# Optimization experiments

Measured on AMD Instinct MI355X. Metric: run time of the kernel, lower is better.

The kernel has to match this reference:

```python
import jax, jax.numpy as jnp
import numpy as np

N_NODES = 100000
N_EDGES = 1600000
NFEAT, NHID, NOUT = 128, 64, 32


def setup_inputs() -> dict:
    key = jax.random.key(0)
    ks = jax.random.split(key, 8)
    x = jax.random.normal(ks[0], (N_NODES, NFEAT), dtype=jnp.float32)
    adj_vals = jax.random.uniform(ks[1], (N_EDGES,), dtype=jnp.float32)
    W1 = jax.random.normal(ks[2], (NFEAT, NHID), dtype=jnp.float32) * (1.0 / np.sqrt(NFEAT))
    b1 = jnp.zeros((NHID,), dtype=jnp.float32)
    W2 = jax.random.normal(ks[3], (NHID, NOUT), dtype=jnp.float32) * (1.0 / np.sqrt(NHID))
    b2 = jnp.zeros((NOUT,), dtype=jnp.float32)
    edge_src = jax.random.randint(ks[4], (N_EDGES,), 0, N_NODES, dtype=jnp.int32)
    edge_dst = jax.random.randint(ks[5], (N_EDGES,), 0, N_NODES, dtype=jnp.int32)
    return {"x": x, "adj_vals": adj_vals, "W1": W1, "b1": b1, "W2": W2,
            "b2": b2, "edge_src": edge_src, "edge_dst": edge_dst}


def spmm(vals, src, dst, dense, n_nodes):
    # out[i, :] = sum_{e : dst[e]==i} vals[e] * dense[src[e], :]
    gathered = dense[src] * vals[:, None]          # [E, D] gather (memory-bound)
    return jax.ops.segment_sum(gathered, dst, num_segments=n_nodes)


def reference(x, adj_vals, W1, b1, W2, b2, edge_src, edge_dst):
    # GraphConvolution 1: support = x @ W1; out = adj @ support + b1; relu
    h = spmm(adj_vals, edge_src, edge_dst, x @ W1, N_NODES) + b1
    h = jax.nn.relu(h)
    # dropout is identity in eval mode (training=False)
    # GraphConvolution 2
    out = spmm(adj_vals, edge_src, edge_dst, h @ W2, N_NODES) + b2
    return out
```

## Files before the change

### kernel.cpp

```cpp
#include <hip/hip_runtime.h>
#include <hip/hip_fp16.h>

#define N_NODES 100000
#define N_EDGES 1600000
#define NFEAT 128
#define NHID 64
#define NOUT 32

#define NPB 256
#define NB ((N_NODES + NPB - 1) / NPB)
#define CAP 4608
#define CCH 4096
#define NCH ((N_EDGES + CCH - 1) / CCH)
#define G1B ((N_NODES / 16 + 3) / 4)

typedef _Float16 half8 __attribute__((ext_vector_type(8)));
typedef float floatx4 __attribute__((ext_vector_type(4)));

__device__ __forceinline__ int wave_incl_scan(int v, int lane) {
#pragma unroll
    for (int d = 1; d < 64; d <<= 1) {
        int t = __shfl_up(v, d, 64);
        if (lane >= d) v += t;
    }
    return v;
}
__device__ __forceinline__ int block_excl_scan_256(int tsum, int tid, int* w4) {
    const int lane = tid & 63, wid = tid >> 6;
    int incl = wave_incl_scan(tsum, lane);
    if (lane == 63) w4[wid] = incl;
    __syncthreads();
    int wbase = 0;
    if (wid > 0) wbase += w4[0];
    if (wid > 1) wbase += w4[1];
    if (wid > 2) wbase += w4[2];
    return wbase + incl - tsum;
}

__global__ __launch_bounds__(64) void prep_kernel(const float* __restrict__ W1,
                                                  __half* __restrict__ wfrag,
                                                  int* __restrict__ gcur) {
    const int l = threadIdx.x;
    const int b = blockIdx.x;
    if (b < 16) {
        const int ks = b >> 2, ct = b & 3;
        const int kb = ks * 32 + (l >> 4) * 8;
        const int c  = ct * 16 + (l & 15);
        union { __half2 h2[4]; uint4 u; } pk;
#pragma unroll
        for (int j = 0; j < 4; ++j)
            pk.h2[j] = __floats2half2_rn(W1[(kb + 2 * j) * NHID + c],
                                         W1[(kb + 2 * j + 1) * NHID + c]);
        *(uint4*)&wfrag[((size_t)b * 64 + l) * 8] = pk.u;
    } else {
        int i = (b - 16) * 64 + l;
        if (i < NB) gcur[i] = i * CAP;
    }
}

__global__ __launch_bounds__(256) void g1cs_kernel(const float* __restrict__ x,
                                                   const __half* __restrict__ wfrag,
                                                   __half* __restrict__ support,
                                                   const float* __restrict__ vals,
                                                   const int* __restrict__ src,
                                                   const int* __restrict__ dst,
                                                   int* __restrict__ gcur,
                                                   uint2* __restrict__ recsC) {
    __shared__ int cnt[NB];
    __shared__ int pos[NB];
    const int tid = threadIdx.x;

    if (blockIdx.x < NCH) {
        const int cbase0 = blockIdx.x * CCH;
        for (int i = tid; i < NB; i += 256) cnt[i] = 0;
        int dstv[CCH / 256];
        __syncthreads();
#pragma unroll
        for (int k = 0; k < CCH / 256; ++k) {
            int e = cbase0 + k * 256 + tid;
            int d = (e < N_EDGES) ? dst[e] : -1;
            dstv[k] = d;
            if (d >= 0) atomicAdd(&cnt[d >> 8], 1);
        }
        __syncthreads();
        for (int b = tid; b < NB; b += 256) {
            int c = cnt[b];
            pos[b] = c ? atomicAdd(&gcur[b], c) : 0;
        }
        __syncthreads();
#pragma unroll
        for (int k = 0; k < CCH / 256; ++k) {
            int e = cbase0 + k * 256 + tid;
            int d = dstv[k];
            if (d >= 0) {
                int b = d >> 8;
                int slot = atomicAdd(&pos[b], 1);
                if (slot < (b + 1) * CAP)
                    recsC[slot] = make_uint2((unsigned)src[e] |
                                             ((unsigned)(d & (NPB - 1)) << 17),
                                             __float_as_uint(vals[e]));
            }
        }
    } else {
        const int lane = tid & 63;
        const int tile = (blockIdx.x - NCH) * 4 + (tid >> 6);
        const int n0 = tile * 16;
        if (n0 >= N_NODES) return;

        half8 a[4][4];
#pragma unroll
        for (int ks = 0; ks < 4; ++ks)
#pragma unroll
            for (int ct = 0; ct < 4; ++ct)
                a[ks][ct] = *(const half8*)&wfrag[((size_t)(ks * 4 + ct) * 64 + lane) * 8];

        floatx4 acc[4];
#pragma unroll
        for (int ct = 0; ct < 4; ++ct) acc[ct] = (floatx4){0.f, 0.f, 0.f, 0.f};

        const int node = n0 + (lane & 15);
        const float* xrow = x + (size_t)node * NFEAT + (lane >> 4) * 8;

#pragma unroll
        for (int ks = 0; ks < 4; ++ks) {
            float4 f0 = *(const float4*)(xrow + ks * 32);
            float4 f1 = *(const float4*)(xrow + ks * 32 + 4);
            union { __half2 h2[4]; half8 v; } bv;
            bv.h2[0] = __floats2half2_rn(f0.x, f0.y);
            bv.h2[1] = __floats2half2_rn(f0.z, f0.w);
            bv.h2[2] = __floats2half2_rn(f1.x, f1.y);
            bv.h2[3] = __floats2half2_rn(f1.z, f1.w);
#pragma unroll
            for (int ct = 0; ct < 4; ++ct)
                acc[ct] = __builtin_amdgcn_mfma_f32_16x16x32_f16(a[ks][ct], bv.v, acc[ct], 0, 0, 0);
        }

        __half* srow = support + (size_t)node * NHID + (lane >> 4) * 4;
#pragma unroll
        for (int ct = 0; ct < 4; ++ct) {
            union { __half2 h2[2]; uint2 u; } pk;
            pk.h2[0] = __floats2half2_rn(acc[ct][0], acc[ct][1]);
            pk.h2[1] = __floats2half2_rn(acc[ct][2], acc[ct][3]);
            *(uint2*)&srow[ct * 16] = pk.u;
        }
    }
}

__global__ __launch_bounds__(256) void fine_sort_kernel(const int* __restrict__ gcur,
                                                        const uint2* __restrict__ recsC,
                                                        uint2* __restrict__ recs2,
                                                        int* __restrict__ offs,
                                                        int* __restrict__ ends) {
    __shared__ int cnt[NPB];
    __shared__ int cur[NPB];
    __shared__ int w4[4];
    const int tid = threadIdx.x;
    const int b = blockIdx.x;
    const int s = b * CAP;
    const int e = min(gcur[b], s + CAP);
    cnt[tid] = 0;
    __syncthreads();
    for (int i = s + tid; i < e; i += 256)
        atomicAdd(&cnt[(recsC[i].x >> 17) & (NPB - 1)], 1);
    __syncthreads();
    int v = cnt[tid];
    int excl = block_excl_scan_256(v, tid, w4);
    cur[tid] = excl;
    const int node = b * NPB + tid;
    if (node < N_NODES) {
        offs[node] = s + excl;
        ends[node] = s + excl + v;
    }
    __syncthreads();
    for (int i = s + tid; i < e; i += 256) {
        uint2 r = recsC[i];
        int dl = (r.x >> 17) & (NPB - 1);
        int p = atomicAdd(&cur[dl], 1);
        recs2[s + p] = make_uint2(r.x & 0x1FFFF, r.y);
    }
}

__global__ __launch_bounds__(256) void spmm1_kernel(const int* __restrict__ offs,
                                                    const int* __restrict__ ends,
                                                    const uint2* __restrict__ recs,
                                                    const __half* __restrict__ dense,
                                                    const float* __restrict__ b1,
                                                    __half* __restrict__ h) {
    __shared__ float red[4][8][65];
    const int tid = threadIdx.x;
    const int lane = tid & 63;
    const int wid = tid >> 6;
    const int d = blockIdx.x * 4 + wid;
    if (d >= N_NODES) return;
    const int g = lane >> 3, q = lane & 7;
    float acc[8];
#pragma unroll
    for (int j = 0; j < 8; ++j) acc[j] = 0.f;

    const int start = offs[d], end = ends[d];
    for (int e = start + g; e < end; e += 8) {
        uint2 r = recs[e];
        float v = __uint_as_float(r.y);
        union { uint4 u; __half2 h2[4]; } rw;
        rw.u = *(const uint4*)((const char*)dense + ((size_t)r.x << 7) + (q << 4));
#pragma unroll
        for (int j = 0; j < 4; ++j) {
            float2 f = __half22float2(rw.h2[j]);
            acc[2 * j]     += v * f.x;
            acc[2 * j + 1] += v * f.y;
        }
    }
#pragma unroll
    for (int j = 0; j < 8; ++j) red[wid][g][q * 8 + j] = acc[j];
    __builtin_amdgcn_wave_barrier();
    float s = 0.f;
#pragma unroll
    for (int gg = 0; gg < 8; ++gg) s += red[wid][gg][lane];
    float hv = fmaxf(s + b1[lane], 0.f);
    h[(size_t)d * NHID + lane] = __float2half(hv);
}

__global__ __launch_bounds__(256) void gemm2_kernel(const __half* __restrict__ h,
                                                    const float* __restrict__ W2,
                                                    __half* __restrict__ s2) {
    __shared__ float wlds[NHID * NOUT];
    const int tid = threadIdx.x;
    for (int i = tid; i < NHID * NOUT; i += 256) wlds[i] = W2[i];

    const int cg = (tid & 7) * 4;
    const int ng = tid >> 3;
    const int n0 = blockIdx.x * 128 + ng * 4;

    int nidx[4];
#pragma unroll
    for (int i = 0; i < 4; ++i) {
        int n = n0 + i;
        nidx[i] = (n < N_NODES) ? n : (N_NODES - 1);
    }
    __syncthreads();

    float acc[4][4];
#pragma unroll
    for (int i = 0; i < 4; ++i)
#pragma unroll
        for (int j = 0; j < 4; ++j) acc[i][j] = 0.f;

    for (int k0 = 0; k0 < NHID; k0 += 8) {
        float hx[4][8];
#pragma unroll
        for (int i = 0; i < 4; ++i) {
            union { float4 f4; __half2 h2[4]; } u;
            u.f4 = *(const float4*)&h[(size_t)nidx[i] * NHID + k0];
#pragma unroll
            for (int j = 0; j < 4; ++j) {
                float2 f = __half22float2(u.h2[j]);
                hx[i][j * 2]     = f.x;
                hx[i][j * 2 + 1] = f.y;
            }
        }
#pragma unroll
        for (int kk = 0; kk < 8; ++kk) {
            float4 w = *(const float4*)&wlds[(k0 + kk) * NOUT + cg];
#pragma unroll
            for (int i = 0; i < 4; ++i) {
                float xv = hx[i][kk];
                acc[i][0] += w.x * xv; acc[i][1] += w.y * xv;
                acc[i][2] += w.z * xv; acc[i][3] += w.w * xv;
            }
        }
    }
#pragma unroll
    for (int i = 0; i < 4; ++i) {
        int n = n0 + i;
        if (n < N_NODES) {
            union { __half2 h2[2]; uint2 u; } pk;
            pk.h2[0] = __floats2half2_rn(acc[i][0], acc[i][1]);
            pk.h2[1] = __floats2half2_rn(acc[i][2], acc[i][3]);
            *(uint2*)&s2[(size_t)n * NOUT + cg] = pk.u;
        }
    }
}

__global__ __launch_bounds__(256) void spmm2_kernel(const int* __restrict__ offs,
                                                    const int* __restrict__ ends,
                                                    const uint2* __restrict__ recs,
                                                    const __half* __restrict__ dense,
                                                    const float* __restrict__ b2,
                                                    float* __restrict__ out) {
    __shared__ float red[4][16][33];
    const int tid = threadIdx.x;
    const int lane = tid & 63;
    const int wid = tid >> 6;
    const int d = blockIdx.x * 4 + wid;
    if (d >= N_NODES) return;
    const int g = lane >> 2, q = lane & 3;
    float acc[8];
#pragma unroll
    for (int j = 0; j < 8; ++j) acc[j] = 0.f;

    const int start = offs[d], end = ends[d];
    for (int e = start + g; e < end; e += 16) {
        uint2 r = recs[e];
        float v = __uint_as_float(r.y);
        union { uint4 u; __half2 h2[4]; } rw;
        rw.u = *(const uint4*)((const char*)dense + ((size_t)r.x << 6) + (q << 4));
#pragma unroll
        for (int j = 0; j < 4; ++j) {
            float2 f = __half22float2(rw.h2[j]);
            acc[2 * j]     += v * f.x;
            acc[2 * j + 1] += v * f.y;
        }
    }
#pragma unroll
    for (int j = 0; j < 8; ++j) red[wid][g][q * 8 + j] = acc[j];
    __builtin_amdgcn_wave_barrier();
    const int f = lane & 31, hi = lane >> 5;
    float s = 0.f;
#pragma unroll
    for (int t = 0; t < 8; ++t) s += red[wid][hi * 8 + t][f];
    s += __shfl_xor(s, 32, 64);
    if (hi == 0) out[(size_t)d * NOUT + f] = s + b2[f];
}

extern "C" void kernel_launch(void* const* d_in, const int* in_sizes, int n_in,
                              void* d_out, int out_size, void* d_ws, size_t ws_size,
                              hipStream_t stream) {
    const float* x        = (const float*)d_in[0];
    const float* adj_vals = (const float*)d_in[1];
    const float* W1       = (const float*)d_in[2];
    const float* b1       = (const float*)d_in[3];
    const float* W2       = (const float*)d_in[4];
    const float* b2       = (const float*)d_in[5];
    const int*   esrc     = (const int*)d_in[6];
    const int*   edst     = (const int*)d_in[7];
    float*       out      = (float*)d_out;

    char* W = (char*)d_ws;
    __half* support = (__half*)W;
    __half* h       = (__half*)(W + 12800000);
    uint2*  recsC   = (uint2*)(W + 25600000);
    uint2*  recs2   = (uint2*)(W + 25600000 + (size_t)NB * CAP * 8);
    int*    IW      = (int*)(W + 25600000 + 2 * (size_t)NB * CAP * 8);
    int*    offs    = IW;
    int*    ends    = IW + 100032;
    int*    gcur    = IW + 200064;
    __half* wfrag   = (__half*)(IW + 200064 + 512);
    __half* s2      = support;

    prep_kernel<<<16 + (NB + 63) / 64, 64, 0, stream>>>(W1, wfrag, gcur);

    g1cs_kernel<<<NCH + G1B, 256, 0, stream>>>(x, wfrag, support,
                                               adj_vals, esrc, edst, gcur, recsC);

    fine_sort_kernel<<<NB, 256, 0, stream>>>(gcur, recsC, recs2, offs, ends);

    spmm1_kernel<<<(N_NODES + 3) / 4, 256, 0, stream>>>(offs, ends, recs2,
                                                        support, b1, h);

    gemm2_kernel<<<(N_NODES + 127) / 128, 256, 0, stream>>>(h, W2, s2);

    spmm2_kernel<<<(N_NODES + 3) / 4, 256, 0, stream>>>(offs, ends, recs2,
                                                        s2, b2, out);
}
```

Measured before the change: 143.6 us.

## Use MFMA for second GEMM and packed half2 FMA accumulation in SpMM

The second dense projection (h @ W2) moves from a scalar FP32 LDS-tiled loop to 16x16x32 f16 MFMA instructions, with W2 pre-packed into fragment layout in the prep kernel. Both SpMM kernels now accumulate per-lane partial sums in packed half2 via hfma2 rather than converting to float and doing scalar FMAs. The aim is fewer ALU instructions in both stages. The risk is lower accuracy from FP16 accumulation over about 16 edges per node, and possible half overflow or rounding error.

```diff
diff --git a/kernel.cpp b/kernel.cpp
--- a/kernel.cpp
+++ b/kernel.cpp
@@ -38,7 +38,9 @@
 }
 
 __global__ __launch_bounds__(64) void prep_kernel(const float* __restrict__ W1,
+                                                  const float* __restrict__ W2,
                                                   __half* __restrict__ wfrag,
+                                                  __half* __restrict__ w2frag,
                                                   int* __restrict__ gcur) {
     const int l = threadIdx.x;
     const int b = blockIdx.x;
@@ -52,8 +54,19 @@
             pk.h2[j] = __floats2half2_rn(W1[(kb + 2 * j) * NHID + c],
                                          W1[(kb + 2 * j + 1) * NHID + c]);
         *(uint4*)&wfrag[((size_t)b * 64 + l) * 8] = pk.u;
+    } else if (b < 20) {
+        const int bb = b - 16;
+        const int ks = bb >> 1, ct = bb & 1;
+        const int kb = ks * 32 + (l >> 4) * 8;
+        const int c  = ct * 16 + (l & 15);
+        union { __half2 h2[4]; uint4 u; } pk;
+#pragma unroll
+        for (int j = 0; j < 4; ++j)
+            pk.h2[j] = __floats2half2_rn(W2[(kb + 2 * j) * NOUT + c],
+                                         W2[(kb + 2 * j + 1) * NOUT + c]);
+        *(uint4*)&w2frag[((size_t)bb * 64 + l) * 8] = pk.u;
     } else {
-        int i = (b - 16) * 64 + l;
+        int i = (b - 20) * 64 + l;
         if (i < NB) gcur[i] = i * CAP;
     }
 }
@@ -193,25 +206,26 @@
     const int d = blockIdx.x * 4 + wid;
     if (d >= N_NODES) return;
     const int g = lane >> 3, q = lane & 7;
-    float acc[8];
-#pragma unroll
-    for (int j = 0; j < 8; ++j) acc[j] = 0.f;
+    __half2 hacc[4];
+#pragma unroll
+    for (int j = 0; j < 4; ++j) hacc[j] = __half2half2(__float2half(0.f));
 
     const int start = offs[d], end = ends[d];
     for (int e = start + g; e < end; e += 8) {
         uint2 r = recs[e];
-        float v = __uint_as_float(r.y);
+        __half2 hv2 = __half2half2(__float2half(__uint_as_float(r.y)));
         union { uint4 u; __half2 h2[4]; } rw;
         rw.u = *(const uint4*)((const char*)dense + ((size_t)r.x << 7) + (q << 4));
 #pragma unroll
-        for (int j = 0; j < 4; ++j) {
-            float2 f = __half22float2(rw.h2[j]);
-            acc[2 * j]     += v * f.x;
-            acc[2 * j + 1] += v * f.y;
-        }
-    }
-#pragma unroll
-    for (int j = 0; j < 8; ++j) red[wid][g][q * 8 + j] = acc[j];
+        for (int j = 0; j < 4; ++j)
+            hacc[j] = __hfma2(rw.h2[j], hv2, hacc[j]);
+    }
+#pragma unroll
+    for (int j = 0; j < 4; ++j) {
+        float2 f = __half22float2(hacc[j]);
+        red[wid][g][q * 8 + 2 * j]     = f.x;
+        red[wid][g][q * 8 + 2 * j + 1] = f.y;
+    }
     __builtin_amdgcn_wave_barrier();
     float s = 0.f;
 #pragma unroll
@@ -221,63 +235,42 @@
 }
 
 __global__ __launch_bounds__(256) void gemm2_kernel(const __half* __restrict__ h,
-                                                    const float* __restrict__ W2,
+                                                    const __half* __restrict__ w2frag,
                                                     __half* __restrict__ s2) {
-    __shared__ float wlds[NHID * NOUT];
-    const int tid = threadIdx.x;
-    for (int i = tid; i < NHID * NOUT; i += 256) wlds[i] = W2[i];
-
-    const int cg = (tid & 7) * 4;
-    const int ng = tid >> 3;
-    const int n0 = blockIdx.x * 128 + ng * 4;
-
-    int nidx[4];
-#pragma unroll
-    for (int i = 0; i < 4; ++i) {
-        int n = n0 + i;
-        nidx[i] = (n < N_NODES) ? n : (N_NODES - 1);
-    }
-    __syncthreads();
-
-    float acc[4][4];
-#pragma unroll
-    for (int i = 0; i < 4; ++i)
-#pragma unroll
-        for (int j = 0; j < 4; ++j) acc[i][j] = 0.f;
-
-    for (int k0 = 0; k0 < NHID; k0 += 8) {
-        float hx[4][8];
-#pragma unroll
-        for (int i = 0; i < 4; ++i) {
-            union { float4 f4; __half2 h2[4]; } u;
-            u.f4 = *(const float4*)&h[(size_t)nidx[i] * NHID + k0];
-#pragma unroll
-            for (int j = 0; j < 4; ++j) {
-                float2 f = __half22float2(u.h2[j]);
-                hx[i][j * 2]     = f.x;
-                hx[i][j * 2 + 1] = f.y;
-            }
-        }
-#pragma unroll
-        for (int kk = 0; kk < 8; ++kk) {
-            float4 w = *(const float4*)&wlds[(k0 + kk) * NOUT + cg];
-#pragma unroll
-            for (int i = 0; i < 4; ++i) {
-                float xv = hx[i][kk];
-                acc[i][0] += w.x * xv; acc[i][1] += w.y * xv;
-                acc[i][2] += w.z * xv; acc[i][3] += w.w * xv;
-            }
-        }
-    }
-#pragma unroll
-    for (int i = 0; i < 4; ++i) {
-        int n = n0 + i;
-        if (n < N_NODES) {
-            union { __half2 h2[2]; uint2 u; } pk;
-            pk.h2[0] = __floats2half2_rn(acc[i][0], acc[i][1]);
-            pk.h2[1] = __floats2half2_rn(acc[i][2], acc[i][3]);
-            *(uint2*)&s2[(size_t)n * NOUT + cg] = pk.u;
-        }
+    const int lane = threadIdx.x & 63;
+    const int tile = blockIdx.x * 4 + (threadIdx.x >> 6);
+    const int n0 = tile * 16;
+    if (n0 >= N_NODES) return;
+
+    half8 a[2][2];
+#pragma unroll
+    for (int ks = 0; ks < 2; ++ks)
+#pragma unroll
+        for (int ct = 0; ct < 2; ++ct)
+            a[ks][ct] = *(const half8*)&w2frag[((size_t)(ks * 2 + ct) * 64 + lane) * 8];
+
+    floatx4 acc[2];
+#pragma unroll
+    for (int ct = 0; ct < 2; ++ct) acc[ct] = (floatx4){0.f, 0.f, 0.f, 0.f};
+
+    const int node = n0 + (lane & 15);
+    const __half* hrow = h + (size_t)node * NHID + (lane >> 4) * 8;
+
+#pragma unroll
+    for (int ks = 0; ks < 2; ++ks) {
+        half8 bv = *(const half8*)(hrow + ks * 32);
+#pragma unroll
+        for (int ct = 0; ct < 2; ++ct)
+            acc[ct] = __builtin_amdgcn_mfma_f32_16x16x32_f16(a[ks][ct], bv, acc[ct], 0, 0, 0);
+    }
+
+    __half* srow = s2 + (size_t)node * NOUT + (lane >> 4) * 4;
+#pragma unroll
+    for (int ct = 0; ct < 2; ++ct) {
+        union { __half2 h2[2]; uint2 u; } pk;
+        pk.h2[0] = __floats2half2_rn(acc[ct][0], acc[ct][1]);
+        pk.h2[1] = __floats2half2_rn(acc[ct][2], acc[ct][3]);
+        *(uint2*)&srow[ct * 16] = pk.u;
     }
 }
 
@@ -294,25 +287,26 @@
     const int d = blockIdx.x * 4 + wid;
     if (d >= N_NODES) return;
     const int g = lane >> 2, q = lane & 3;
-    float acc[8];
-#pragma unroll
-    for (int j = 0; j < 8; ++j) acc[j] = 0.f;
+    __half2 hacc[4];
+#pragma unroll
+    for (int j = 0; j < 4; ++j) hacc[j] = __half2half2(__float2half(0.f));
 
     const int start = offs[d], end = ends[d];
     for (int e = start + g; e < end; e += 16) {
         uint2 r = recs[e];
-        float v = __uint_as_float(r.y);
+        __half2 hv2 = __half2half2(__float2half(__uint_as_float(r.y)));
         union { uint4 u; __half2 h2[4]; } rw;
         rw.u = *(const uint4*)((const char*)dense + ((size_t)r.x << 6) + (q << 4));
 #pragma unroll
-        for (int j = 0; j < 4; ++j) {
-            float2 f = __half22float2(rw.h2[j]);
-            acc[2 * j]     += v * f.x;
-            acc[2 * j + 1] += v * f.y;
-        }
-    }
-#pragma unroll
-    for (int j = 0; j < 8; ++j) red[wid][g][q * 8 + j] = acc[j];
+        for (int j = 0; j < 4; ++j)
+            hacc[j] = __hfma2(rw.h2[j], hv2, hacc[j]);
+    }
+#pragma unroll
+    for (int j = 0; j < 4; ++j) {
+        float2 f = __half22float2(hacc[j]);
+        red[wid][g][q * 8 + 2 * j]     = f.x;
+        red[wid][g][q * 8 + 2 * j + 1] = f.y;
+    }
     __builtin_amdgcn_wave_barrier();
     const int f = lane & 31, hi = lane >> 5;
     float s = 0.f;
@@ -345,9 +339,10 @@
     int*    ends    = IW + 100032;
     int*    gcur    = IW + 200064;
     __half* wfrag   = (__half*)(IW + 200064 + 512);
+    __half* w2frag  = wfrag + 8192;
     __half* s2      = support;
 
-    prep_kernel<<<16 + (NB + 63) / 64, 64, 0, stream>>>(W1, wfrag, gcur);
+    prep_kernel<<<20 + (NB + 63) / 64, 64, 0, stream>>>(W1, W2, wfrag, w2frag, gcur);
 
     g1cs_kernel<<<NCH + G1B, 256, 0, stream>>>(x, wfrag, support,
                                                adj_vals, esrc, edst, gcur, recsC);
@@ -357,7 +352,7 @@
     spmm1_kernel<<<(N_NODES + 3) / 4, 256, 0, stream>>>(offs, ends, recs2,
                                                         support, b1, h);
 
-    gemm2_kernel<<<(N_NODES + 127) / 128, 256, 0, stream>>>(h, W2, s2);
+    gemm2_kernel<<<(N_NODES / 16 + 3) / 4, 256, 0, stream>>>(h, w2frag, s2);
 
     spmm2_kernel<<<(N_NODES + 3) / 4, 256, 0, stream>>>(offs, ends, recs2,
                                                         s2, b2, out);
```

New measurement: 136.4 us. 1.05x faster.
